# Performance work log

Hardware: AMD Instinct MI355X
Metric: run time of the kernel (lower is better)

The kernel has to match this reference:

```python
import jax, jax.numpy as jnp
import numpy as np

E, C, H, W = 64, 8, 32, 32  # E zonotope rows (1 center + 63 error terms)


def setup_inputs() -> dict:
    key = jax.random.key(0)
    x = jax.random.normal(key, (E, C, H, W), dtype=jnp.float32)
    # Zero center => lower < 0 < upper everywhere, so every element crosses
    # and the number of new error terms equals C*H*W (fixed output shape).
    x = x.at[0].set(0.0)
    return {"x": x}


def reference(x):
    e = x.shape[0]
    content_shape = x.shape[1:]
    n = int(np.prod(content_shape))  # max possible new error terms

    err = jnp.sum(jnp.abs(x[1:]), axis=0)
    upper = x[0] + err
    lower = x[0] - err

    cross = (lower * upper < 0).astype(x.dtype)   # crossing-zero mask
    nonneg = (lower >= 0).astype(x.dtype)         # strictly positive mask

    lam = nonneg + cross * upper / (upper - lower)
    lam = jnp.where(jnp.isnan(lam), 0.5, lam)
    # torch assigns lambda via .data (detached from the autograd graph)
    lam = jax.lax.stop_gradient(lam)

    delta = jnp.maximum(-lam * lower, (1.0 - lam) * upper)

    head = (delta / 2 + lam * x[0]) * cross + x[0] * nonneg          # new center
    body = x[1:] * (lam * cross + nonneg)                            # scaled old error terms

    # Vectorized stream-compaction scatter replacing the scripted .item() loop:
    # element k (flat order) with cross==True goes to tail row cumsum(cross)[k]-1.
    flat_cond = cross.reshape(-1) > 0
    vals = (delta / 2).reshape(-1)
    rows = jnp.cumsum(flat_cond.astype(jnp.int32)) - 1
    rows = jnp.clip(rows, 0, n - 1)
    tail = jnp.zeros((n, n), dtype=x.dtype)
    # (row, col) pairs are unique per column; masked-out elements write 0 (no-op).
    tail = tail.at[rows, jnp.arange(n)].set(jnp.where(flat_cond, vals, 0.0))

    return jnp.concatenate(
        [head[None], body, tail.reshape((n,) + content_shape)], axis=0
    )
```

## Files before the change

### kernel.cpp

```cpp
#include <hip/hip_runtime.h>
#include <math.h>

#define EROWS 64
#define NCOL  8192
#define TAIL_OFF (EROWS * NCOL)
#define TAIL_F4 (NCOL * NCOL / 4)
#define ROW_F4  (NCOL / 4)

#define WS_VAL(ws)     ((float*)(ws))
#define WS_FLAG(ws)    ((int*)((char*)(ws) + 32768))
#define WS_COLOF(ws)   ((int*)((char*)(ws) + 65536))
#define WS_TAILVAL(ws) ((float*)((char*)(ws) + 98304))
#define WS_COUNT(ws)   ((int*)((char*)(ws) + 131072))

__global__ void headbody_kernel(const float* __restrict__ x,
                                float* __restrict__ out,
                                float* __restrict__ val,
                                int* __restrict__ flag) {
    int k = blockIdx.x * blockDim.x + threadIdx.x;
    if (k >= NCOL) return;

    float err = 0.f;
    for (int e = 1; e < EROWS; ++e)
        err += fabsf(x[e * NCOL + k]);

    float x0    = x[k];
    float upper = x0 + err;
    float lower = x0 - err;

    float cross  = (lower * upper < 0.f) ? 1.f : 0.f;
    float nonneg = (lower >= 0.f) ? 1.f : 0.f;

    float lam = nonneg + cross * upper / (upper - lower);
    if (isnan(lam)) lam = 0.5f;

    float delta = fmaxf(-lam * lower, (1.f - lam) * upper);

    out[k] = (delta * 0.5f + lam * x0) * cross + x0 * nonneg;

    float scale = lam * cross + nonneg;
    val[k]  = delta * 0.5f;
    flag[k] = (cross > 0.f) ? 1 : 0;

    for (int e = 1; e < EROWS; ++e)
        out[e * NCOL + k] = x[e * NCOL + k] * scale;
}

__global__ void scan_kernel(const float* __restrict__ val,
                            const int* __restrict__ flag,
                            int* __restrict__ colof,
                            float* __restrict__ tailval,
                            int* __restrict__ count) {
    const int t = threadIdx.x;
    const int PER = NCOL / 1024;

    int f[PER];
    int s = 0;
    for (int j = 0; j < PER; ++j) {
        f[j] = flag[t * PER + j];
        s += f[j];
    }

    __shared__ int sh[1024];
    sh[t] = s;
    __syncthreads();

    for (int off = 1; off < 1024; off <<= 1) {
        int v = (t >= off) ? sh[t - off] : 0;
        __syncthreads();
        sh[t] += v;
        __syncthreads();
    }
    int running = (t == 0) ? 0 : sh[t - 1];

    for (int j = 0; j < PER; ++j) {
        int k = t * PER + j;
        if (f[j]) {
            colof[running]   = k;
            tailval[running] = val[k];
            ++running;
        }
    }
    if (t == 1023) *count = sh[1023];
}

__global__ void tail_kernel(const int* __restrict__ colof,
                            const float* __restrict__ tailval,
                            const int* __restrict__ count,
                            float* __restrict__ out) {
    int q  = blockIdx.x * blockDim.x + threadIdx.x;
    int r  = q >> 11;
    int c0 = (q & 2047) << 2;

    int cnt = *count;
    int   col = (r < cnt) ? colof[r]   : -1;
    float tv  = (r < cnt) ? tailval[r] : 0.f;

    float4 v;
    v.x = (col == c0 + 0) ? tv : 0.f;
    v.y = (col == c0 + 1) ? tv : 0.f;
    v.z = (col == c0 + 2) ? tv : 0.f;
    v.w = (col == c0 + 3) ? tv : 0.f;

    ((float4*)out)[TAIL_OFF / 4 + q] = v;
}

extern "C" void kernel_launch(void* const* d_in, const int* in_sizes, int n_in,
                              void* d_out, int out_size, void* d_ws, size_t ws_size,
                              hipStream_t stream) {
    const float* x = (const float*)d_in[0];
    float* out = (float*)d_out;

    headbody_kernel<<<NCOL / 256, 256, 0, stream>>>(x, out, WS_VAL(d_ws), WS_FLAG(d_ws));
    scan_kernel<<<1, 1024, 0, stream>>>(WS_VAL(d_ws), WS_FLAG(d_ws),
                                        WS_COLOF(d_ws), WS_TAILVAL(d_ws), WS_COUNT(d_ws));
    tail_kernel<<<TAIL_F4 / 256, 256, 0, stream>>>(WS_COLOF(d_ws), WS_TAILVAL(d_ws),
                                                   WS_COUNT(d_ws), out);
}
```

Measured before the change: 273.2 us.

## Use wave-shuffle scan, smaller headbody blocks, and multi-row tail writer blocks

The headbody kernel now runs 64-thread blocks with its row loops unrolled, which spreads the 8192 columns across 128 blocks instead of 32. The scan replaces the shared-memory Hillis-Steele scan and its many barriers with a wave-level shuffle scan plus per-wave sums, and loads its flags as int4. The tail kernel has each block write four full rows, eight float4 stores per thread per row, which cuts the block count and reuses one index lookup per row. The 256 MB tail write still dominates, so the gains from the smaller kernels are likely marginal.

```diff
diff --git a/kernel.cpp b/kernel.cpp
--- a/kernel.cpp
+++ b/kernel.cpp
@@ -13,14 +13,14 @@
 #define WS_TAILVAL(ws) ((float*)((char*)(ws) + 98304))
 #define WS_COUNT(ws)   ((int*)((char*)(ws) + 131072))
 
-__global__ void headbody_kernel(const float* __restrict__ x,
+__global__ __launch_bounds__(64) void headbody_kernel(const float* __restrict__ x,
                                 float* __restrict__ out,
                                 float* __restrict__ val,
                                 int* __restrict__ flag) {
-    int k = blockIdx.x * blockDim.x + threadIdx.x;
-    if (k >= NCOL) return;
+    int k = blockIdx.x * 64 + threadIdx.x;
 
     float err = 0.f;
+#pragma unroll
     for (int e = 1; e < EROWS; ++e)
         err += fabsf(x[e * NCOL + k]);
 
@@ -42,67 +42,81 @@
     val[k]  = delta * 0.5f;
     flag[k] = (cross > 0.f) ? 1 : 0;
 
+#pragma unroll
     for (int e = 1; e < EROWS; ++e)
         out[e * NCOL + k] = x[e * NCOL + k] * scale;
 }
 
-__global__ void scan_kernel(const float* __restrict__ val,
+__global__ __launch_bounds__(1024) void scan_kernel(const float* __restrict__ val,
                             const int* __restrict__ flag,
                             int* __restrict__ colof,
                             float* __restrict__ tailval,
                             int* __restrict__ count) {
-    const int t = threadIdx.x;
-    const int PER = NCOL / 1024;
+    const int t    = threadIdx.x;
+    const int lane = t & 63;
+    const int wid  = t >> 6;
 
-    int f[PER];
+    int4 a = ((const int4*)flag)[t * 2 + 0];
+    int4 b = ((const int4*)flag)[t * 2 + 1];
+    int f[8] = {a.x, a.y, a.z, a.w, b.x, b.y, b.z, b.w};
+
     int s = 0;
-    for (int j = 0; j < PER; ++j) {
-        f[j] = flag[t * PER + j];
-        s += f[j];
+#pragma unroll
+    for (int j = 0; j < 8; ++j) s += f[j];
+
+    int isc = s;
+#pragma unroll
+    for (int off = 1; off < 64; off <<= 1) {
+        int v = __shfl_up(isc, off);
+        if (lane >= off) isc += v;
     }
 
-    __shared__ int sh[1024];
-    sh[t] = s;
+    __shared__ int wsum[16];
+    if (lane == 63) wsum[wid] = isc;
     __syncthreads();
 
-    for (int off = 1; off < 1024; off <<= 1) {
-        int v = (t >= off) ? sh[t - off] : 0;
-        __syncthreads();
-        sh[t] += v;
-        __syncthreads();
-    }
-    int running = (t == 0) ? 0 : sh[t - 1];
+    int base = 0;
+    for (int w = 0; w < wid; ++w) base += wsum[w];
 
-    for (int j = 0; j < PER; ++j) {
-        int k = t * PER + j;
+    int running = base + isc - s;
+    const int kbase = t * 8;
+#pragma unroll
+    for (int j = 0; j < 8; ++j) {
         if (f[j]) {
-            colof[running]   = k;
-            tailval[running] = val[k];
+            colof[running]   = kbase + j;
+            tailval[running] = val[kbase + j];
             ++running;
         }
     }
-    if (t == 1023) *count = sh[1023];
+    if (t == 1023) *count = base + isc;
 }
 
-__global__ void tail_kernel(const int* __restrict__ colof,
-                            const float* __restrict__ tailval,
-                            const int* __restrict__ count,
-                            float* __restrict__ out) {
-    int q  = blockIdx.x * blockDim.x + threadIdx.x;
-    int r  = q >> 11;
-    int c0 = (q & 2047) << 2;
+__global__ __launch_bounds__(256) void tail_kernel(const int* __restrict__ colof,
+                           const float* __restrict__ tailval,
+                           const int* __restrict__ count,
+                           float* __restrict__ out) {
+    const int t    = threadIdx.x;
+    const int row0 = blockIdx.x * 4;
+    const int cnt  = *count;
+    float4* tail = (float4*)out + TAIL_OFF / 4;
 
-    int cnt = *count;
-    int   col = (r < cnt) ? colof[r]   : -1;
-    float tv  = (r < cnt) ? tailval[r] : 0.f;
-
-    float4 v;
-    v.x = (col == c0 + 0) ? tv : 0.f;
-    v.y = (col == c0 + 1) ? tv : 0.f;
-    v.z = (col == c0 + 2) ? tv : 0.f;
-    v.w = (col == c0 + 3) ? tv : 0.f;
-
-    ((float4*)out)[TAIL_OFF / 4 + q] = v;
+#pragma unroll
+    for (int j = 0; j < 4; ++j) {
+        int   r   = row0 + j;
+        int   col = (r < cnt) ? colof[r]   : -1;
+        float tv  = (r < cnt) ? tailval[r] : 0.f;
+        float4* rowp = tail + (size_t)r * ROW_F4;
+#pragma unroll
+        for (int i = 0; i < 8; ++i) {
+            int c0 = (t + i * 256) << 2;
+            float4 v;
+            v.x = (col == c0 + 0) ? tv : 0.f;
+            v.y = (col == c0 + 1) ? tv : 0.f;
+            v.z = (col == c0 + 2) ? tv : 0.f;
+            v.w = (col == c0 + 3) ? tv : 0.f;
+            rowp[t + i * 256] = v;
+        }
+    }
 }
 
 extern "C" void kernel_launch(void* const* d_in, const int* in_sizes, int n_in,
@@ -111,9 +125,9 @@
     const float* x = (const float*)d_in[0];
     float* out = (float*)d_out;
 
-    headbody_kernel<<<NCOL / 256, 256, 0, stream>>>(x, out, WS_VAL(d_ws), WS_FLAG(d_ws));
+    headbody_kernel<<<NCOL / 64, 64, 0, stream>>>(x, out, WS_VAL(d_ws), WS_FLAG(d_ws));
     scan_kernel<<<1, 1024, 0, stream>>>(WS_VAL(d_ws), WS_FLAG(d_ws),
                                         WS_COLOF(d_ws), WS_TAILVAL(d_ws), WS_COUNT(d_ws));
-    tail_kernel<<<TAIL_F4 / 256, 256, 0, stream>>>(WS_COLOF(d_ws), WS_TAILVAL(d_ws),
-                                                   WS_COUNT(d_ws), out);
+    tail_kernel<<<NCOL / 4, 256, 0, stream>>>(WS_COLOF(d_ws), WS_TAILVAL(d_ws),
+                                              WS_COUNT(d_ws), out);
 }
```

Result: no change. 271.6 us (-0.6%).
